# Kernel tuning notes

Measured on AMD Instinct MI355X. Metric: run time of the kernel, lower is better.

The kernel has to match this reference:

```python
import jax, jax.numpy as jnp
import numpy as np

B, N, DIM, HEADS, DIM_HEAD = 2, 2048, 1024, 16, 64
SCALE = DIM_HEAD ** -0.5


def setup_inputs() -> dict:
    key = jax.random.key(0)
    k1, k2, k3, k4, k5 = jax.random.split(key, 5)
    x = jax.random.normal(k1, (B, N, DIM), dtype=jnp.float32)
    causal_boundary_indices = jax.random.randint(k2, (B,), 0, N)
    # Parameters
    Wq = jax.random.normal(k3, (HEADS, DIM, DIM_HEAD), dtype=jnp.float32) * (DIM ** -0.5)
    Wkv = jax.random.normal(k4, (DIM, 2 * DIM_HEAD), dtype=jnp.float32) * (DIM ** -0.5)
    Wo = jax.random.normal(k5, (HEADS * DIM_HEAD, DIM), dtype=jnp.float32) * ((HEADS * DIM_HEAD) ** -0.5)
    return {"x": x, "Wq": Wq, "Wkv": Wkv, "Wo": Wo,
            "causal_boundary_indices": causal_boundary_indices}


def reference(x, Wq, Wkv, Wo, causal_boundary_indices):
    b, n, d = x.shape
    # Multi-query attention: per-head Q, single shared K/V head
    q = jnp.einsum('bnd,hde->bhne', x, Wq) * SCALE          # [b,h,n,dh]
    kv = x @ Wkv                                            # [b,n,2*dh]
    k, v = jnp.split(kv, 2, axis=-1)                        # [b,n,dh] each
    sim = jnp.einsum('bhid,bjd->bhij', q, k)                # [b,h,n,n]
    max_neg = -jnp.finfo(sim.dtype).max
    seq = jnp.arange(n)
    causal_mask = seq[None, :] > seq[:, None]               # [n,n] True = masked
    # positions j < boundary[b] are fully visible (prefix-LM); only j >= boundary obey causality
    mask_after = seq[None, None, None, :] >= causal_boundary_indices[:, None, None, None]
    mask = causal_mask[None, None, :, :] & mask_after       # [b,1,n,n]
    sim = jnp.where(mask, max_neg, sim)
    attn = jax.nn.softmax(sim, axis=-1)
    out = jnp.einsum('bhij,bjd->bhid', attn, v)             # [b,h,n,dh]
    out = out.transpose(0, 2, 1, 3).reshape(b, n, -1)       # [b,n,h*dh]
    return out @ Wo                                         # [b,n,d]
```

## Files before the change

kernel.cpp:

```cpp
#include <hip/hip_runtime.h>
#include <hip/hip_bf16.h>

typedef unsigned short ushort_t;
typedef unsigned int u32;
typedef __attribute__((ext_vector_type(8))) short bf16x8;
typedef __attribute__((ext_vector_type(4))) float f32x4;
typedef __attribute__((ext_vector_type(16))) float f32x16;
typedef __attribute__((ext_vector_type(2))) unsigned int u32x2;

#define L2E 1.44269504f

__device__ __forceinline__ ushort_t f2bf(float f) {
    union { __hip_bfloat16 b; ushort_t u; } c;
    c.b = __float2bfloat16(f);
    return c.u;
}

__device__ __forceinline__ f32x4 mfma16(bf16x8 a, bf16x8 b, f32x4 c) {
    return __builtin_amdgcn_mfma_f32_16x16x32_bf16(a, b, c, 0, 0, 0);
}

__device__ __forceinline__ f32x16 mfma32(bf16x8 a, bf16x8 b, f32x16 c) {
    return __builtin_amdgcn_mfma_f32_32x32x16_bf16(a, b, c, 0, 0, 0);
}

__device__ __forceinline__ u32 cvtpk(float lo, float hi) {
    u32 r;
    asm("v_cvt_pk_bf16_f32 %0, %1, %2" : "=v"(r) : "v"(lo), "v"(hi));
    return r;
}

__device__ __forceinline__ u32x2 pl32swap(u32 a, u32 b) {
#if __has_builtin(__builtin_amdgcn_permlane32_swap)
    auto r = __builtin_amdgcn_permlane32_swap((int)a, (int)b, false, false);
    return u32x2{(u32)r[0], (u32)r[1]};
#else
    u32 sa = (u32)__shfl_xor((int)a, 32);
    u32 sb = (u32)__shfl_xor((int)b, 32);
    int lane = threadIdx.x & 63;
    u32 d = (lane >= 32) ? sb : a;
    u32 s = (lane >= 32) ? b : sa;
    return u32x2{d, s};
#endif
}

__device__ __forceinline__ float swap32f(float x, int hi) {
    union { float f; u32 u; } c; c.f = x;
    u32x2 r = pl32swap(c.u, c.u);
    union { u32 u; float f; } o; o.u = hi ? r[0] : r[1];
    return o.f;
}

__device__ __forceinline__ void gload_lds16(const ushort_t* g, ushort_t* l) {
    __builtin_amdgcn_global_load_lds(
        (const __attribute__((address_space(1))) unsigned int*)g,
        (__attribute__((address_space(3))) unsigned int*)l, 16, 0, 0);
}


__global__ __launch_bounds__(256)
void convert_kernel(const float* __restrict__ x, const float* __restrict__ Wq,
                    const float* __restrict__ Wkv, const float* __restrict__ Wo,
                    ushort_t* __restrict__ Xbf, ushort_t* __restrict__ W1bt,
                    ushort_t* __restrict__ Wobt) {
    int idx = blockIdx.x * 256 + threadIdx.x;
    if (idx < 4194304) { Xbf[idx] = f2bf(x[idx]); return; }
    idx -= 4194304;
    if (idx < 1179648) {
        int c = idx >> 10, d = idx & 1023;
        float v;
        if (c < 1024) v = Wq[((size_t)((c >> 6) * 1024 + d)) * 64 + (c & 63)] * 0.125f;
        else          v = Wkv[(size_t)d * 128 + (c - 1024)];
        W1bt[idx] = f2bf(v);
        return;
    }
    idx -= 1179648;
    if (idx < 1048576) {
        int j = idx >> 10, i = idx & 1023;
        Wobt[idx] = f2bf(Wo[(size_t)i * 1024 + j]);
    }
}

template <int MODE>
__global__ __launch_bounds__(256)
void gemm128(const ushort_t* __restrict__ A, const ushort_t* __restrict__ Bt,
             ushort_t* __restrict__ Cq, ushort_t* __restrict__ Ck,
             ushort_t* __restrict__ Cv, float* __restrict__ Cf, int K) {
    __shared__ ushort_t As[128][72];
    __shared__ ushort_t Bs[128][72];
    const int tid = threadIdx.x;
    const int lane = tid & 63;
    const int w = tid >> 6;
    const int wm = w >> 1, wn = w & 1;
    const int l15 = lane & 15, g = lane >> 4;
    const int tm = blockIdx.x, tn = blockIdx.y;

    f32x4 acc[4][4];
#pragma unroll
    for (int i = 0; i < 4; i++)
#pragma unroll
        for (int j = 0; j < 4; j++) acc[i][j] = (f32x4)(0.f);

    const int srow = tid >> 3, sseg = tid & 7;
    const ushort_t* Ag = A + ((size_t)(tm * 128 + srow)) * K + sseg * 8;
    const ushort_t* Bg = Bt + ((size_t)(tn * 128 + srow)) * K + sseg * 8;

    bf16x8 ra[4], rb[4];
#pragma unroll
    for (int i = 0; i < 4; i++) {
        ra[i] = *(const bf16x8*)(Ag + (size_t)i * 32 * K);
        rb[i] = *(const bf16x8*)(Bg + (size_t)i * 32 * K);
    }
    const int nk = K >> 6;
    for (int kt = 0; kt < nk; ++kt) {
        __syncthreads();
#pragma unroll
        for (int i = 0; i < 4; i++) {
            *(bf16x8*)&As[srow + i * 32][sseg * 8] = ra[i];
            *(bf16x8*)&Bs[srow + i * 32][sseg * 8] = rb[i];
        }
        __syncthreads();
        if (kt + 1 < nk) {
            const ushort_t* Ag2 = Ag + (kt + 1) * 64;
            const ushort_t* Bg2 = Bg + (kt + 1) * 64;
#pragma unroll
            for (int i = 0; i < 4; i++) {
                ra[i] = *(const bf16x8*)(Ag2 + (size_t)i * 32 * K);
                rb[i] = *(const bf16x8*)(Bg2 + (size_t)i * 32 * K);
            }
        }
#pragma unroll
        for (int kc = 0; kc < 2; kc++) {
            bf16x8 af[4], bfr[4];
#pragma unroll
            for (int mi = 0; mi < 4; mi++)
                af[mi] = *(const bf16x8*)&As[wm * 64 + mi * 16 + l15][kc * 32 + 8 * g];
#pragma unroll
            for (int ni = 0; ni < 4; ni++)
                bfr[ni] = *(const bf16x8*)&Bs[wn * 64 + ni * 16 + l15][kc * 32 + 8 * g];
#pragma unroll
            for (int mi = 0; mi < 4; mi++)
#pragma unroll
                for (int ni = 0; ni < 4; ni++)
                    acc[mi][ni] = mfma16(af[mi], bfr[ni], acc[mi][ni]);
        }
    }
#pragma unroll
    for (int mi = 0; mi < 4; mi++)
#pragma unroll
        for (int ni = 0; ni < 4; ni++)
#pragma unroll
            for (int r = 0; r < 4; r++) {
                int row = tm * 128 + wm * 64 + mi * 16 + 4 * g + r;
                int col = tn * 128 + wn * 64 + ni * 16 + l15;
                float v = acc[mi][ni][r];
                if (MODE == 0) {
                    if (col < 1024) {
                        Cq[(size_t)row * 1024 + col] = f2bf(v);
                    } else if (col < 1088) {
                        int e = col - 1024;
                        int n = row & 2047, bb = row >> 11;
                        int t = n >> 6;
                        int idx = t * 4096 + (((n >> 5) & 1) * 4 + (e >> 4)) * 512 +
                                  (((e >> 3) & 1) * 32 + (n & 31)) * 8 + (e & 7);
                        Ck[(size_t)bb * 131072 + idx] = f2bf(v);
                    } else {
                        int d = col - 1088;
                        int n = row & 2047, bb = row >> 11;
                        int t = n >> 6;
                        int idx = t * 4096 + ((d >> 5) * 4 + ((n >> 4) & 3)) * 512 +
                                  (((n >> 3) & 1) * 32 + (d & 31)) * 8 + (n & 7);
                        Cv[(size_t)bb * 131072 + idx] = f2bf(v);
                    }
                } else {
                    Cf[(size_t)row * 1024 + col] = v;
                }
            }
}

__global__ __launch_bounds__(256, 2)
void attn32(const ushort_t* __restrict__ Qb, const ushort_t* __restrict__ Kt,
            const ushort_t* __restrict__ Vt2, ushort_t* __restrict__ Ob,
            const int* __restrict__ bnds) {
    __shared__ ushort_t sK[2][4096];
    __shared__ ushort_t sV[2][4096];
    const int tid = threadIdx.x;
    const int lane = tid & 63;
    const int w = tid >> 6;
    const int l31 = lane & 31;
    const int hi = lane >> 5;

    const int id = blockIdx.x;
    const int s = id & 255;
    const int flip = id >> 8;
    const int b = s >> 7;
    const int qt5 = (s >> 2) & 31;
    const int hg = s & 3;
    const int qt = flip ? 63 - qt5 : qt5;
    const int h = hg * 4 + w;
    const int bnd = bnds[b];
    const int qbase = qt * 32;
    const int q = qbase + l31;

    const ushort_t* Qp = Qb + ((size_t)(b * 2048 + q)) * 1024 + h * 64 + hi * 8;
    bf16x8 Qf[4];
#pragma unroll
    for (int kk = 0; kk < 4; kk++) Qf[kk] = *(const bf16x8*)(Qp + kk * 16);

    f32x16 oacc0 = (f32x16)(0.f), oacc1 = (f32x16)(0.f);
    float m = -3e38f, lsum = 0.f;

    int wl = qbase + 31;
    if (bnd - 1 > wl) wl = bnd - 1;
    if (wl > 2047) wl = 2047;
    const int niter = (wl >> 6) + 1;

    const ushort_t* Kglob = Kt + (size_t)b * 131072;
    const ushort_t* Vglob = Vt2 + (size_t)b * 131072;

    auto stage = [&](int buf, int t) {
        if (w < 2) {
            const ushort_t* g = Kglob + (size_t)t * 4096 + (w * 4) * 512 + lane * 8;
            ushort_t* l = &sK[buf][(w * 4) * 512];
#pragma unroll
            for (int j = 0; j < 4; j++) gload_lds16(g + j * 512, l + j * 512);
        } else {
            const ushort_t* g = Vglob + (size_t)t * 4096 + ((w - 2) * 4) * 512 + lane * 8;
            ushort_t* l = &sV[buf][((w - 2) * 4) * 512];
#pragma unroll
            for (int j = 0; j < 4; j++) gload_lds16(g + j * 512, l + j * 512);
        }
    };

    stage(0, 0);
    asm volatile("s_waitcnt vmcnt(0)" ::: "memory");
    __syncthreads();

    int cur = 0;
    for (int it = 0; it < niter; ++it) {
        const int k0 = it * 64;
        if (it + 1 < niter) stage(cur ^ 1, it + 1);

        bf16x8 kfr[8];
#pragma unroll
        for (int r = 0; r < 8; r++)
            kfr[r] = *(const bf16x8*)&sK[cur][r * 512 + lane * 8];
        f32x16 s0 = (f32x16)(0.f), s1 = (f32x16)(0.f);
        __builtin_amdgcn_s_setprio(1);
#pragma unroll
        for (int kk = 0; kk < 4; kk++) {
            s0 = mfma32(kfr[kk], Qf[kk], s0);
            s1 = mfma32(kfr[4 + kk], Qf[kk], s1);
        }
        __builtin_amdgcn_s_setprio(0);

        const bool fullvis = (k0 + 63 <= qbase) || (k0 + 63 < bnd);
        if (!fullvis) {
#pragma unroll
            for (int r = 0; r < 16; r++) {
                int key0 = k0 + (r & 3) + 8 * (r >> 2) + 4 * hi;
                if (key0 > q && key0 >= bnd) s0[r] = -3e38f;
                int key1 = key0 + 32;
                if (key1 > q && key1 >= bnd) s1[r] = -3e38f;
            }
        }

        float tmax = fmaxf(s0[0], s0[1]);
#pragma unroll
        for (int r = 2; r < 16; r++) tmax = fmaxf(tmax, s0[r]);
#pragma unroll
        for (int r = 0; r < 16; r++) tmax = fmaxf(tmax, s1[r]);
        tmax = fmaxf(tmax, swap32f(tmax, hi));

        if (!__all(tmax <= m + 8.0f)) {
            float mnew = fmaxf(m, tmax);
            float alpha = __builtin_amdgcn_exp2f((m - mnew) * L2E);
#pragma unroll
            for (int r = 0; r < 16; r++) { oacc0[r] *= alpha; oacc1[r] *= alpha; }
            lsum *= alpha;
            m = mnew;
        }
        const float mL = m * L2E;

        bf16x8 vfr[8];
#pragma unroll
        for (int r = 0; r < 8; r++)
            vfr[r] = *(const bf16x8*)&sV[cur][r * 512 + lane * 8];

        __builtin_amdgcn_s_setprio(1);
#pragma unroll
        for (int c = 0; c < 4; c++) {
            float p0, p1, p2, p3, p4, p5, p6, p7;
            {
                const f32x16& sc = (c < 2) ? s0 : s1;
                const int base = (c & 1) * 8;
                p0 = __builtin_amdgcn_exp2f(sc[base + 0] * L2E - mL);
                p1 = __builtin_amdgcn_exp2f(sc[base + 1] * L2E - mL);
                p2 = __builtin_amdgcn_exp2f(sc[base + 2] * L2E - mL);
                p3 = __builtin_amdgcn_exp2f(sc[base + 3] * L2E - mL);
                p4 = __builtin_amdgcn_exp2f(sc[base + 4] * L2E - mL);
                p5 = __builtin_amdgcn_exp2f(sc[base + 5] * L2E - mL);
                p6 = __builtin_amdgcn_exp2f(sc[base + 6] * L2E - mL);
                p7 = __builtin_amdgcn_exp2f(sc[base + 7] * L2E - mL);
            }
            lsum += ((p0 + p1) + (p2 + p3)) + ((p4 + p5) + (p6 + p7));
            u32 a0 = cvtpk(p0, p1);
            u32 c0 = cvtpk(p2, p3);
            u32 b0 = cvtpk(p4, p5);
            u32 d0 = cvtpk(p6, p7);
            u32x2 r02 = pl32swap(a0, b0);
            u32x2 r13 = pl32swap(c0, d0);
            union { u32 u[4]; bf16x8 v; } P;
            P.u[0] = r02[0]; P.u[1] = r13[0]; P.u[2] = r02[1]; P.u[3] = r13[1];
            oacc0 = mfma32(vfr[c], P.v, oacc0);
            oacc1 = mfma32(vfr[4 + c], P.v, oacc1);
        }
        __builtin_amdgcn_s_setprio(0);

        asm volatile("s_waitcnt vmcnt(0)" ::: "memory");
        __syncthreads();
        cur ^= 1;
    }

    const float ltot = lsum + swap32f(lsum, hi);
    const float li = 1.f / ltot;
    ushort_t* Op = Ob + ((size_t)(b * 2048 + q)) * 1024 + h * 64;
#pragma unroll
    for (int dh = 0; dh < 2; dh++)
#pragma unroll
        for (int rq = 0; rq < 4; rq++) {
            union { ushort_t s[4]; u32x2 u; } st;
#pragma unroll
            for (int j = 0; j < 4; j++) {
                float v = (dh == 0 ? oacc0[4 * rq + j] : oacc1[4 * rq + j]) * li;
                st.s[j] = f2bf(v);
            }
            int d0 = dh * 32 + 8 * rq + 4 * hi;
            *(u32x2*)(Op + d0) = st.u;
        }
}

extern "C" void kernel_launch(void* const* d_in, const int* in_sizes, int n_in,
                              void* d_out, int out_size, void* d_ws, size_t ws_size,
                              hipStream_t stream) {
    const float* x   = (const float*)d_in[0];
    const float* Wq  = (const float*)d_in[1];
    const float* Wkv = (const float*)d_in[2];
    const float* Wo  = (const float*)d_in[3];
    const int* bnds  = (const int*)d_in[4];
    char* ws = (char*)d_ws;
    ushort_t* Xbf  = (ushort_t*)(ws);
    ushort_t* W1bt = (ushort_t*)(ws + 8388608);
    ushort_t* Wobt = (ushort_t*)(ws + 10747904);
    ushort_t* Qb   = (ushort_t*)(ws + 12845056);
    ushort_t* Kb   = (ushort_t*)(ws + 21233664);
    ushort_t* Vt   = (ushort_t*)(ws + 21757952);
    ushort_t* Ob   = (ushort_t*)(ws + 22282240);
    float* out = (float*)d_out;

    convert_kernel<<<dim3(25088), dim3(256), 0, stream>>>(x, Wq, Wkv, Wo, Xbf, W1bt, Wobt);
    gemm128<0><<<dim3(32, 9), dim3(256), 0, stream>>>(Xbf, W1bt, Qb, Kb, Vt, (float*)nullptr, 1024);
    attn32<<<dim3(512), dim3(256), 0, stream>>>(Qb, Kb, Vt, Ob, bnds);
    gemm128<1><<<dim3(32, 8), dim3(256), 0, stream>>>(Ob, Wobt, (ushort_t*)nullptr,
                                                      (ushort_t*)nullptr, (ushort_t*)nullptr, out, 1024);
}
```

Baseline: 104.6 us.

## Split attention KV sequence across two wave groups with LDS merge

Doubles the attention block to 512 threads so that two groups of four waves each process alternating 64-key tiles for the same query tile and heads. Both tiles are staged per round into a larger shared buffer, and at the end the second group writes its partial accumulators, max and sum to LDS, which the first group merges with log-sum-exp rescaling before writing output. This halves the serial loop length per wave and adds latency hiding, at the cost of more registers per CU pressure, more LDS (64KB), a final merge sync, and idle waves on odd tile counts.

```diff
diff --git a/kernel.cpp b/kernel.cpp
--- a/kernel.cpp
+++ b/kernel.cpp
@@ -178,17 +178,18 @@
             }
 }
 
-__global__ __launch_bounds__(256, 2)
+__global__ __launch_bounds__(512, 4)
 void attn32(const ushort_t* __restrict__ Qb, const ushort_t* __restrict__ Kt,
             const ushort_t* __restrict__ Vt2, ushort_t* __restrict__ Ob,
             const int* __restrict__ bnds) {
-    __shared__ ushort_t sK[2][4096];
-    __shared__ ushort_t sV[2][4096];
+    __shared__ ushort_t smem[2][16384];
     const int tid = threadIdx.x;
     const int lane = tid & 63;
     const int w = tid >> 6;
     const int l31 = lane & 31;
     const int hi = lane >> 5;
+    const int split = w >> 2;
+    const int hw = w & 3;
 
     const int id = blockIdx.x;
     const int s = id & 255;
@@ -197,7 +198,7 @@
     const int qt5 = (s >> 2) & 31;
     const int hg = s & 3;
     const int qt = flip ? 63 - qt5 : qt5;
-    const int h = hg * 4 + w;
+    const int h = hg * 4 + hw;
     const int bnd = bnds[b];
     const int qbase = qt * 32;
     const int q = qbase + l31;
@@ -214,22 +215,20 @@
     if (bnd - 1 > wl) wl = bnd - 1;
     if (wl > 2047) wl = 2047;
     const int niter = (wl >> 6) + 1;
+    const int nrounds = (niter + 1) >> 1;
 
     const ushort_t* Kglob = Kt + (size_t)b * 131072;
     const ushort_t* Vglob = Vt2 + (size_t)b * 131072;
 
-    auto stage = [&](int buf, int t) {
-        if (w < 2) {
-            const ushort_t* g = Kglob + (size_t)t * 4096 + (w * 4) * 512 + lane * 8;
-            ushort_t* l = &sK[buf][(w * 4) * 512];
-#pragma unroll
-            for (int j = 0; j < 4; j++) gload_lds16(g + j * 512, l + j * 512);
-        } else {
-            const ushort_t* g = Vglob + (size_t)t * 4096 + ((w - 2) * 4) * 512 + lane * 8;
-            ushort_t* l = &sV[buf][((w - 2) * 4) * 512];
-#pragma unroll
-            for (int j = 0; j < 4; j++) gload_lds16(g + j * 512, l + j * 512);
-        }
+    const int stp = w >> 2, skv = (w >> 1) & 1, shf = w & 1;
+    const ushort_t* sgbase = (skv ? Vglob : Kglob) + shf * 2048 + lane * 8;
+    const int sldst = stp * 8192 + skv * 4096 + shf * 2048;
+    auto stage = [&](int buf, int r) {
+        int t = 2 * r + stp;
+        const ushort_t* g = sgbase + (size_t)t * 4096;
+        ushort_t* l = &smem[buf][sldst];
+#pragma unroll
+        for (int j = 0; j < 4; j++) gload_lds16(g + j * 512, l + j * 512);
     };
 
     stage(0, 0);
@@ -237,85 +236,90 @@
     __syncthreads();
 
     int cur = 0;
-    for (int it = 0; it < niter; ++it) {
-        const int k0 = it * 64;
-        if (it + 1 < niter) stage(cur ^ 1, it + 1);
-
-        bf16x8 kfr[8];
-#pragma unroll
-        for (int r = 0; r < 8; r++)
-            kfr[r] = *(const bf16x8*)&sK[cur][r * 512 + lane * 8];
-        f32x16 s0 = (f32x16)(0.f), s1 = (f32x16)(0.f);
-        __builtin_amdgcn_s_setprio(1);
-#pragma unroll
-        for (int kk = 0; kk < 4; kk++) {
-            s0 = mfma32(kfr[kk], Qf[kk], s0);
-            s1 = mfma32(kfr[4 + kk], Qf[kk], s1);
+    for (int r = 0; r < nrounds; ++r) {
+        if (r + 1 < nrounds) stage(cur ^ 1, r + 1);
+        const int t = 2 * r + split;
+        if (t < niter) {
+            const int k0 = t * 64;
+            const ushort_t* kb = &smem[cur][split * 8192];
+            const ushort_t* vb = kb + 4096;
+
+            bf16x8 kfr[8];
+#pragma unroll
+            for (int r8 = 0; r8 < 8; r8++)
+                kfr[r8] = *(const bf16x8*)&kb[r8 * 512 + lane * 8];
+            f32x16 s0 = (f32x16)(0.f), s1 = (f32x16)(0.f);
+            __builtin_amdgcn_s_setprio(1);
+#pragma unroll
+            for (int kk = 0; kk < 4; kk++) {
+                s0 = mfma32(kfr[kk], Qf[kk], s0);
+                s1 = mfma32(kfr[4 + kk], Qf[kk], s1);
+            }
+            __builtin_amdgcn_s_setprio(0);
+
+            const bool fullvis = (k0 + 63 <= qbase) || (k0 + 63 < bnd);
+            if (!fullvis) {
+#pragma unroll
+                for (int rr = 0; rr < 16; rr++) {
+                    int key0 = k0 + (rr & 3) + 8 * (rr >> 2) + 4 * hi;
+                    if (key0 > q && key0 >= bnd) s0[rr] = -3e38f;
+                    int key1 = key0 + 32;
+                    if (key1 > q && key1 >= bnd) s1[rr] = -3e38f;
+                }
+            }
+
+            float tmax = fmaxf(s0[0], s0[1]);
+#pragma unroll
+            for (int rr = 2; rr < 16; rr++) tmax = fmaxf(tmax, s0[rr]);
+#pragma unroll
+            for (int rr = 0; rr < 16; rr++) tmax = fmaxf(tmax, s1[rr]);
+            tmax = fmaxf(tmax, swap32f(tmax, hi));
+
+            if (!__all(tmax <= m + 8.0f)) {
+                float mnew = fmaxf(m, tmax);
+                float alpha = __builtin_amdgcn_exp2f((m - mnew) * L2E);
+#pragma unroll
+                for (int rr = 0; rr < 16; rr++) { oacc0[rr] *= alpha; oacc1[rr] *= alpha; }
+                lsum *= alpha;
+                m = mnew;
+            }
+            const float mL = m * L2E;
+
+            bf16x8 vfr[8];
+#pragma unroll
+            for (int r8 = 0; r8 < 8; r8++)
+                vfr[r8] = *(const bf16x8*)&vb[r8 * 512 + lane * 8];
+
+            __builtin_amdgcn_s_setprio(1);
+#pragma unroll
+            for (int c = 0; c < 4; c++) {
+                float p0, p1, p2, p3, p4, p5, p6, p7;
+                {
+                    const f32x16& sc = (c < 2) ? s0 : s1;
+                    const int base = (c & 1) * 8;
+                    p0 = __builtin_amdgcn_exp2f(sc[base + 0] * L2E - mL);
+                    p1 = __builtin_amdgcn_exp2f(sc[base + 1] * L2E - mL);
+                    p2 = __builtin_amdgcn_exp2f(sc[base + 2] * L2E - mL);
+                    p3 = __builtin_amdgcn_exp2f(sc[base + 3] * L2E - mL);
+                    p4 = __builtin_amdgcn_exp2f(sc[base + 4] * L2E - mL);
+                    p5 = __builtin_amdgcn_exp2f(sc[base + 5] * L2E - mL);
+                    p6 = __builtin_amdgcn_exp2f(sc[base + 6] * L2E - mL);
+                    p7 = __builtin_amdgcn_exp2f(sc[base + 7] * L2E - mL);
+                }
+                lsum += ((p0 + p1) + (p2 + p3)) + ((p4 + p5) + (p6 + p7));
+                u32 a0 = cvtpk(p0, p1);
+                u32 c0 = cvtpk(p2, p3);
+                u32 b0 = cvtpk(p4, p5);
+                u32 d0 = cvtpk(p6, p7);
+                u32x2 r02 = pl32swap(a0, b0);
+                u32x2 r13 = pl32swap(c0, d0);
+                union { u32 u[4]; bf16x8 v; } P;
+                P.u[0] = r02[0]; P.u[1] = r13[0]; P.u[2] = r02[1]; P.u[3] = r13[1];
+                oacc0 = mfma32(vfr[c], P.v, oacc0);
+                oacc1 = mfma32(vfr[4 + c], P.v, oacc1);
+            }
+            __builtin_amdgcn_s_setprio(0);
         }
-        __builtin_amdgcn_s_setprio(0);
-
-        const bool fullvis = (k0 + 63 <= qbase) || (k0 + 63 < bnd);
-        if (!fullvis) {
-#pragma unroll
-            for (int r = 0; r < 16; r++) {
-                int key0 = k0 + (r & 3) + 8 * (r >> 2) + 4 * hi;
-                if (key0 > q && key0 >= bnd) s0[r] = -3e38f;
-                int key1 = key0 + 32;
-                if (key1 > q && key1 >= bnd) s1[r] = -3e38f;
-            }
-        }
-
-        float tmax = fmaxf(s0[0], s0[1]);
-#pragma unroll
-        for (int r = 2; r < 16; r++) tmax = fmaxf(tmax, s0[r]);
-#pragma unroll
-        for (int r = 0; r < 16; r++) tmax = fmaxf(tmax, s1[r]);
-        tmax = fmaxf(tmax, swap32f(tmax, hi));
-
-        if (!__all(tmax <= m + 8.0f)) {
-            float mnew = fmaxf(m, tmax);
-            float alpha = __builtin_amdgcn_exp2f((m - mnew) * L2E);
-#pragma unroll
-            for (int r = 0; r < 16; r++) { oacc0[r] *= alpha; oacc1[r] *= alpha; }
-            lsum *= alpha;
-            m = mnew;
-        }
-        const float mL = m * L2E;
-
-        bf16x8 vfr[8];
-#pragma unroll
-        for (int r = 0; r < 8; r++)
-            vfr[r] = *(const bf16x8*)&sV[cur][r * 512 + lane * 8];
-
-        __builtin_amdgcn_s_setprio(1);
-#pragma unroll
-        for (int c = 0; c < 4; c++) {
-            float p0, p1, p2, p3, p4, p5, p6, p7;
-            {
-                const f32x16& sc = (c < 2) ? s0 : s1;
-                const int base = (c & 1) * 8;
-                p0 = __builtin_amdgcn_exp2f(sc[base + 0] * L2E - mL);
-                p1 = __builtin_amdgcn_exp2f(sc[base + 1] * L2E - mL);
-                p2 = __builtin_amdgcn_exp2f(sc[base + 2] * L2E - mL);
-                p3 = __builtin_amdgcn_exp2f(sc[base + 3] * L2E - mL);
-                p4 = __builtin_amdgcn_exp2f(sc[base + 4] * L2E - mL);
-                p5 = __builtin_amdgcn_exp2f(sc[base + 5] * L2E - mL);
-                p6 = __builtin_amdgcn_exp2f(sc[base + 6] * L2E - mL);
-                p7 = __builtin_amdgcn_exp2f(sc[base + 7] * L2E - mL);
-            }
-            lsum += ((p0 + p1) + (p2 + p3)) + ((p4 + p5) + (p6 + p7));
-            u32 a0 = cvtpk(p0, p1);
-            u32 c0 = cvtpk(p2, p3);
-            u32 b0 = cvtpk(p4, p5);
-            u32 d0 = cvtpk(p6, p7);
-            u32x2 r02 = pl32swap(a0, b0);
-            u32x2 r13 = pl32swap(c0, d0);
-            union { u32 u[4]; bf16x8 v; } P;
-            P.u[0] = r02[0]; P.u[1] = r13[0]; P.u[2] = r02[1]; P.u[3] = r13[1];
-            oacc0 = mfma32(vfr[c], P.v, oacc0);
-            oacc1 = mfma32(vfr[4 + c], P.v, oacc1);
-        }
-        __builtin_amdgcn_s_setprio(0);
 
         asm volatile("s_waitcnt vmcnt(0)" ::: "memory");
         __syncthreads();
@@ -323,21 +327,41 @@
     }
 
     const float ltot = lsum + swap32f(lsum, hi);
-    const float li = 1.f / ltot;
-    ushort_t* Op = Ob + ((size_t)(b * 2048 + q)) * 1024 + h * 64;
-#pragma unroll
-    for (int dh = 0; dh < 2; dh++)
-#pragma unroll
-        for (int rq = 0; rq < 4; rq++) {
-            union { ushort_t s[4]; u32x2 u; } st;
-#pragma unroll
-            for (int j = 0; j < 4; j++) {
-                float v = (dh == 0 ? oacc0[4 * rq + j] : oacc1[4 * rq + j]) * li;
-                st.s[j] = f2bf(v);
-            }
-            int d0 = dh * 32 + 8 * rq + 4 * hi;
-            *(u32x2*)(Op + d0) = st.u;
-        }
+
+    float* mg = (float*)&smem[0][0];
+    if (split == 1) {
+        float* dst = &mg[(hw * 64 + lane) * 34];
+#pragma unroll
+        for (int i = 0; i < 16; i++) { dst[i] = oacc0[i]; dst[16 + i] = oacc1[i]; }
+        dst[32] = m;
+        dst[33] = ltot;
+    }
+    __syncthreads();
+    if (split == 0) {
+        const float* src = &mg[(hw * 64 + lane) * 34];
+        const float mB = src[32], lB = src[33];
+        const float mf = fmaxf(m, mB);
+        const float aA = __builtin_amdgcn_exp2f((m - mf) * L2E);
+        const float aB = __builtin_amdgcn_exp2f((mB - mf) * L2E);
+        const float li = 1.f / (ltot * aA + lB * aB);
+
+        ushort_t* Op = Ob + ((size_t)(b * 2048 + q)) * 1024 + h * 64;
+#pragma unroll
+        for (int dh = 0; dh < 2; dh++)
+#pragma unroll
+            for (int rq = 0; rq < 4; rq++) {
+                union { ushort_t s[4]; u32x2 u; } st;
+#pragma unroll
+                for (int j = 0; j < 4; j++) {
+                    const int idx = 4 * rq + j;
+                    float a = (dh == 0) ? oacc0[idx] : oacc1[idx];
+                    float v = (a * aA + src[dh * 16 + idx] * aB) * li;
+                    st.s[j] = f2bf(v);
+                }
+                int d0 = dh * 32 + 8 * rq + 4 * hi;
+                *(u32x2*)(Op + d0) = st.u;
+            }
+    }
 }
 
 extern "C" void kernel_launch(void* const* d_in, const int* in_sizes, int n_in,
@@ -360,7 +384,7 @@
 
     convert_kernel<<<dim3(25088), dim3(256), 0, stream>>>(x, Wq, Wkv, Wo, Xbf, W1bt, Wobt);
     gemm128<0><<<dim3(32, 9), dim3(256), 0, stream>>>(Xbf, W1bt, Qb, Kb, Vt, (float*)nullptr, 1024);
-    attn32<<<dim3(512), dim3(256), 0, stream>>>(Qb, Kb, Vt, Ob, bnds);
+    attn32<<<dim3(512), dim3(512), 0, stream>>>(Qb, Kb, Vt, Ob, bnds);
     gemm128<1><<<dim3(32, 8), dim3(256), 0, stream>>>(Ob, Wobt, (ushort_t*)nullptr,
                                                       (ushort_t*)nullptr, (ushort_t*)nullptr, out, 1024);
 }
```

After: 110.4 us. 5.6% more time.

## Pre-permute GEMM operands into MFMA tile layout and stream via direct global-to-LDS loads

Applied to the files above, without the earlier changes.

The convert kernel now writes X, W1 and Wo as bf16 in a tile-blocked, fragment-ordered layout, 8 elements per thread with packed conversion. The attention kernel writes its output in the same permuted layout. The GEMMs can then fill double-buffered LDS with global_load_lds and read MFMA fragments contiguously. This aims to remove the register staging, the padded strided LDS stores and the extra sync per k-step, and setprio is added around the MFMAs. In exchange, the strided weight gathers in the convert kernel become less coalesced, and LDS use doubles with two buffers per operand.

```diff
diff --git a/kernel.cpp b/kernel.cpp
--- a/kernel.cpp
+++ b/kernel.cpp
@@ -58,42 +58,74 @@
 }
 
 
+__device__ __forceinline__ int perm_off(int row, int k) {
+    return (((row >> 6) & 1) * 8 + ((row >> 4) & 3) * 2 + ((k >> 5) & 1)) * 512
+         + (row & 15) * 8 + ((k >> 3) & 3) * 128 + (k & 7);
+}
+
 __global__ __launch_bounds__(256)
 void convert_kernel(const float* __restrict__ x, const float* __restrict__ Wq,
                     const float* __restrict__ Wkv, const float* __restrict__ Wo,
-                    ushort_t* __restrict__ Xbf, ushort_t* __restrict__ W1bt,
-                    ushort_t* __restrict__ Wobt) {
+                    ushort_t* __restrict__ Xp, ushort_t* __restrict__ W1p,
+                    ushort_t* __restrict__ Wop) {
     int idx = blockIdx.x * 256 + threadIdx.x;
-    if (idx < 4194304) { Xbf[idx] = f2bf(x[idx]); return; }
-    idx -= 4194304;
-    if (idx < 1179648) {
-        int c = idx >> 10, d = idx & 1023;
-        float v;
-        if (c < 1024) v = Wq[((size_t)((c >> 6) * 1024 + d)) * 64 + (c & 63)] * 0.125f;
-        else          v = Wkv[(size_t)d * 128 + (c - 1024)];
-        W1bt[idx] = f2bf(v);
+    if (idx < 524288) {
+        int row = idx >> 7, k = (idx & 127) << 3;
+        const float* src = x + (size_t)row * 1024 + k;
+        f32x4 a = *(const f32x4*)src, c2 = *(const f32x4*)(src + 4);
+        union { u32 u[4]; bf16x8 v; } P;
+        P.u[0] = cvtpk(a[0], a[1]);  P.u[1] = cvtpk(a[2], a[3]);
+        P.u[2] = cvtpk(c2[0], c2[1]); P.u[3] = cvtpk(c2[2], c2[3]);
+        size_t tile = (size_t)((row >> 7) * 16 + (k >> 6));
+        *(bf16x8*)(Xp + tile * 8192 + perm_off(row, k)) = P.v;
         return;
     }
-    idx -= 1179648;
-    if (idx < 1048576) {
-        int j = idx >> 10, i = idx & 1023;
-        Wobt[idx] = f2bf(Wo[(size_t)i * 1024 + j]);
+    idx -= 524288;
+    if (idx < 147456) {
+        int c = idx >> 7, k = (idx & 127) << 3;
+        float v[8];
+        if (c < 1024) {
+            const float* s = Wq + ((size_t)(c >> 6) * 1024 + k) * 64 + (c & 63);
+#pragma unroll
+            for (int e = 0; e < 8; e++) v[e] = s[(size_t)e * 64] * 0.125f;
+        } else {
+            const float* s = Wkv + (size_t)k * 128 + (c - 1024);
+#pragma unroll
+            for (int e = 0; e < 8; e++) v[e] = s[(size_t)e * 128];
+        }
+        union { u32 u[4]; bf16x8 vv; } P;
+        P.u[0] = cvtpk(v[0], v[1]); P.u[1] = cvtpk(v[2], v[3]);
+        P.u[2] = cvtpk(v[4], v[5]); P.u[3] = cvtpk(v[6], v[7]);
+        size_t tile = (size_t)((c >> 7) * 16 + (k >> 6));
+        *(bf16x8*)(W1p + tile * 8192 + perm_off(c, k)) = P.vv;
+        return;
+    }
+    idx -= 147456;
+    if (idx < 131072) {
+        int j = idx >> 7, k = (idx & 127) << 3;
+        const float* s = Wo + (size_t)k * 1024 + j;
+        float v[8];
+#pragma unroll
+        for (int e = 0; e < 8; e++) v[e] = s[(size_t)e * 1024];
+        union { u32 u[4]; bf16x8 vv; } P;
+        P.u[0] = cvtpk(v[0], v[1]); P.u[1] = cvtpk(v[2], v[3]);
+        P.u[2] = cvtpk(v[4], v[5]); P.u[3] = cvtpk(v[6], v[7]);
+        size_t tile = (size_t)((j >> 7) * 16 + (k >> 6));
+        *(bf16x8*)(Wop + tile * 8192 + perm_off(j, k)) = P.vv;
     }
 }
 
 template <int MODE>
-__global__ __launch_bounds__(256)
-void gemm128(const ushort_t* __restrict__ A, const ushort_t* __restrict__ Bt,
-             ushort_t* __restrict__ Cq, ushort_t* __restrict__ Ck,
-             ushort_t* __restrict__ Cv, float* __restrict__ Cf, int K) {
-    __shared__ ushort_t As[128][72];
-    __shared__ ushort_t Bs[128][72];
-    const int tid = threadIdx.x;
-    const int lane = tid & 63;
-    const int w = tid >> 6;
-    const int wm = w >> 1, wn = w & 1;
-    const int l15 = lane & 15, g = lane >> 4;
+__global__ __launch_bounds__(256, 2)
+void gemmp(const ushort_t* __restrict__ Ap, const ushort_t* __restrict__ Bp,
+           ushort_t* __restrict__ Cq, ushort_t* __restrict__ Ck,
+           ushort_t* __restrict__ Cv, float* __restrict__ Cf) {
+    __shared__ ushort_t sA[2][8192];
+    __shared__ ushort_t sB[2][8192];
+    const int tid = threadIdx.x, lane = tid & 63, w = tid >> 6;
+    const int wm = w >> 1, wn = w & 1, l15 = lane & 15, g = lane >> 4;
     const int tm = blockIdx.x, tn = blockIdx.y;
+    constexpr int KT = 16;
 
     f32x4 acc[4][4];
 #pragma unroll
@@ -101,50 +133,49 @@
 #pragma unroll
         for (int j = 0; j < 4; j++) acc[i][j] = (f32x4)(0.f);
 
-    const int srow = tid >> 3, sseg = tid & 7;
-    const ushort_t* Ag = A + ((size_t)(tm * 128 + srow)) * K + sseg * 8;
-    const ushort_t* Bg = Bt + ((size_t)(tn * 128 + srow)) * K + sseg * 8;
-
-    bf16x8 ra[4], rb[4];
-#pragma unroll
-    for (int i = 0; i < 4; i++) {
-        ra[i] = *(const bf16x8*)(Ag + (size_t)i * 32 * K);
-        rb[i] = *(const bf16x8*)(Bg + (size_t)i * 32 * K);
-    }
-    const int nk = K >> 6;
-    for (int kt = 0; kt < nk; ++kt) {
-        __syncthreads();
-#pragma unroll
-        for (int i = 0; i < 4; i++) {
-            *(bf16x8*)&As[srow + i * 32][sseg * 8] = ra[i];
-            *(bf16x8*)&Bs[srow + i * 32][sseg * 8] = rb[i];
-        }
-        __syncthreads();
-        if (kt + 1 < nk) {
-            const ushort_t* Ag2 = Ag + (kt + 1) * 64;
-            const ushort_t* Bg2 = Bg + (kt + 1) * 64;
-#pragma unroll
-            for (int i = 0; i < 4; i++) {
-                ra[i] = *(const bf16x8*)(Ag2 + (size_t)i * 32 * K);
-                rb[i] = *(const bf16x8*)(Bg2 + (size_t)i * 32 * K);
-            }
-        }
+    const ushort_t* Abase = Ap + (size_t)tm * KT * 8192;
+    const ushort_t* Bbase = Bp + (size_t)tn * KT * 8192;
+
+    auto stage = [&](int buf, int kt) {
+        const ushort_t* ga = Abase + (size_t)kt * 8192 + (w * 4) * 512 + lane * 8;
+        const ushort_t* gb = Bbase + (size_t)kt * 8192 + (w * 4) * 512 + lane * 8;
+        ushort_t* la = &sA[buf][(w * 4) * 512];
+        ushort_t* lb = &sB[buf][(w * 4) * 512];
+#pragma unroll
+        for (int j = 0; j < 4; j++) {
+            gload_lds16(ga + j * 512, la + j * 512);
+            gload_lds16(gb + j * 512, lb + j * 512);
+        }
+    };
+
+    stage(0, 0);
+    asm volatile("s_waitcnt vmcnt(0)" ::: "memory");
+    __syncthreads();
+    int cur = 0;
+    for (int kt = 0; kt < KT; ++kt) {
+        if (kt + 1 < KT) stage(cur ^ 1, kt + 1);
 #pragma unroll
         for (int kc = 0; kc < 2; kc++) {
             bf16x8 af[4], bfr[4];
 #pragma unroll
             for (int mi = 0; mi < 4; mi++)
-                af[mi] = *(const bf16x8*)&As[wm * 64 + mi * 16 + l15][kc * 32 + 8 * g];
+                af[mi] = *(const bf16x8*)&sA[cur][(wm * 8 + mi * 2 + kc) * 512 + lane * 8];
 #pragma unroll
             for (int ni = 0; ni < 4; ni++)
-                bfr[ni] = *(const bf16x8*)&Bs[wn * 64 + ni * 16 + l15][kc * 32 + 8 * g];
+                bfr[ni] = *(const bf16x8*)&sB[cur][(wn * 8 + ni * 2 + kc) * 512 + lane * 8];
+            __builtin_amdgcn_s_setprio(1);
 #pragma unroll
             for (int mi = 0; mi < 4; mi++)
 #pragma unroll
                 for (int ni = 0; ni < 4; ni++)
                     acc[mi][ni] = mfma16(af[mi], bfr[ni], acc[mi][ni]);
-        }
-    }
+            __builtin_amdgcn_s_setprio(0);
+        }
+        asm volatile("s_waitcnt vmcnt(0)" ::: "memory");
+        __syncthreads();
+        cur ^= 1;
+    }
+
 #pragma unroll
     for (int mi = 0; mi < 4; mi++)
 #pragma unroll
@@ -324,7 +355,10 @@
 
     const float ltot = lsum + swap32f(lsum, hi);
     const float li = 1.f / ltot;
-    ushort_t* Op = Ob + ((size_t)(b * 2048 + q)) * 1024 + h * 64;
+
+    const int rowO = b * 2048 + q;
+    const int segbase = ((rowO >> 6) & 1) * 8 + ((rowO >> 4) & 3) * 2;
+    ushort_t* ObT = Ob + ((size_t)(rowO >> 7) * 16 + h) * 8192 + (rowO & 15) * 8 + 4 * hi;
 #pragma unroll
     for (int dh = 0; dh < 2; dh++)
 #pragma unroll
@@ -335,8 +369,7 @@
                 float v = (dh == 0 ? oacc0[4 * rq + j] : oacc1[4 * rq + j]) * li;
                 st.s[j] = f2bf(v);
             }
-            int d0 = dh * 32 + 8 * rq + 4 * hi;
-            *(u32x2*)(Op + d0) = st.u;
+            *(u32x2*)(ObT + (segbase + dh) * 512 + rq * 128) = st.u;
         }
 }
 
@@ -358,9 +391,9 @@
     ushort_t* Ob   = (ushort_t*)(ws + 22282240);
     float* out = (float*)d_out;
 
-    convert_kernel<<<dim3(25088), dim3(256), 0, stream>>>(x, Wq, Wkv, Wo, Xbf, W1bt, Wobt);
-    gemm128<0><<<dim3(32, 9), dim3(256), 0, stream>>>(Xbf, W1bt, Qb, Kb, Vt, (float*)nullptr, 1024);
+    convert_kernel<<<dim3(3136), dim3(256), 0, stream>>>(x, Wq, Wkv, Wo, Xbf, W1bt, Wobt);
+    gemmp<0><<<dim3(32, 9), dim3(256), 0, stream>>>(Xbf, W1bt, Qb, Kb, Vt, (float*)nullptr);
     attn32<<<dim3(512), dim3(256), 0, stream>>>(Qb, Kb, Vt, Ob, bnds);
-    gemm128<1><<<dim3(32, 8), dim3(256), 0, stream>>>(Ob, Wobt, (ushort_t*)nullptr,
-                                                      (ushort_t*)nullptr, (ushort_t*)nullptr, out, 1024);
-}
+    gemmp<1><<<dim3(32, 8), dim3(256), 0, stream>>>(Ob, Wobt, (ushort_t*)nullptr,
+                                                    (ushort_t*)nullptr, (ushort_t*)nullptr, out);
+}
```

After: 110.2 us. +5.3%, slower.
